# Performance work log

Measured on AMD Instinct MI355X. Metric: run time of the kernel, lower is better.

## Reference

```python
import jax, jax.numpy as jnp
import numpy as np
import math

L, B, T, S, D, H = 6, 4, 1024, 1024, 1024, 16
HD = D // H
SCALE = 1.0 / math.sqrt(HD)
EPS = 1e-5


def _ln(x, w, b):
    m = x.mean(-1, keepdims=True)
    v = ((x - m) ** 2).mean(-1, keepdims=True)
    return (x - m) * jax.lax.rsqrt(v + EPS) * w + b


def _mha(xq, xkv, qw, qb, kw, kb, vw, vb, ow, ob, mask):
    b, t, _ = xq.shape
    s = xkv.shape[1]
    q = (xq @ qw.T + qb).reshape(b, t, H, HD).transpose(0, 2, 1, 3)
    k = (xkv @ kw.T + kb).reshape(b, s, H, HD).transpose(0, 2, 1, 3)
    v = (xkv @ vw.T + vb).reshape(b, s, H, HD).transpose(0, 2, 1, 3)
    scores = jnp.einsum('bhqd,bhkd->bhqk', q, k) * SCALE
    scores = jnp.where(mask == 0, -jnp.inf, scores)
    attn = jax.nn.softmax(scores, axis=-1)  # dropout is identity (eval)
    o = jnp.einsum('bhqk,bhkd->bhqd', attn, v).transpose(0, 2, 1, 3).reshape(b, t, D)
    return o @ ow.T + ob


def _ffn(x, f1w, f1b, f2w, f2b, fnw, fnb):
    h = jax.nn.gelu(x @ f1w.T + f1b, approximate=False)
    y = h @ f2w.T + f2b
    return x + _ln(y, fnw, fnb)


def setup_inputs() -> dict:
    key = jax.random.key(0)
    ks = jax.random.split(key, 16)
    wf = lambda k: jax.random.normal(k, (L, D, D), jnp.float32) * 0.02
    zb = jnp.zeros((L, D), jnp.float32)
    ones = jnp.ones((L, D), jnp.float32)
    inp = {
        'x': jax.random.normal(ks[0], (B, T, D), jnp.float32),
        'enc_outputs': jax.random.normal(ks[1], (B, S, D), jnp.float32),
        'sqw': wf(ks[2]), 'sqb': zb, 'skw': wf(ks[3]), 'skb': zb,
        'svw': wf(ks[4]), 'svb': zb, 'sow': wf(ks[5]), 'sob': zb,
        'cqw': wf(ks[6]), 'cqb': zb, 'ckw': wf(ks[7]), 'ckb': zb,
        'cvw': wf(ks[8]), 'cvb': zb, 'cow': wf(ks[9]), 'cob': zb,
        'f1w': wf(ks[10]), 'f1b': zb, 'f2w': wf(ks[11]), 'f2b': zb,
        'fnw': ones, 'fnb': zb,
        'l1w': ones, 'l1b': zb, 'l2w': ones, 'l2b': zb, 'l3w': ones, 'l3b': zb,
        'src_mask': jnp.ones((1, 1, T, S), jnp.int32),
        'tgt_mask': jnp.tril(jnp.ones((T, T), jnp.int32))[None, None],
    }
    return inp


def reference(x, enc_outputs, sqw, sqb, skw, skb, svw, svb, sow, sob,
              cqw, cqb, ckw, ckb, cvw, cvb, cow, cob,
              f1w, f1b, f2w, f2b, fnw, fnb,
              l1w, l1b, l2w, l2b, l3w, l3b, src_mask, tgt_mask):
    for l in range(L):
        sa = _mha(x, x, sqw[l], sqb[l], skw[l], skb[l], svw[l], svb[l], sow[l], sob[l], tgt_mask)
        x = _ln(x + sa, l1w[l], l1b[l])
        ca = _mha(x, enc_outputs, cqw[l], cqb[l], ckw[l], ckb[l], cvw[l], cvb[l], cow[l], cob[l], src_mask)
        x = _ln(x + ca, l2w[l], l2b[l])
        ff = _ffn(x, f1w[l], f1b[l], f2w[l], f2b[l], fnw[l], fnb[l])
        x = _ln(x + ff, l3w[l], l3b[l])
    return x
```

## Files before the change

kernel.cpp:

```cpp
#include <hip/hip_runtime.h>
#include <stdint.h>

typedef unsigned short u16;
typedef unsigned int u32;
typedef __bf16 bf16x8 __attribute__((ext_vector_type(8)));
typedef float f32x4 __attribute__((ext_vector_type(4)));
typedef u16 u16x8 __attribute__((ext_vector_type(8)));
typedef u16 u16x4 __attribute__((ext_vector_type(4)));
typedef u32 u32x2 __attribute__((ext_vector_type(2)));

#define MFMA16(A, B, C) __builtin_amdgcn_mfma_f32_16x16x32_bf16((A), (B), (C), 0, 0, 0)

#define GLOAD_LDS16(GP, LP)                                                    \
  __builtin_amdgcn_global_load_lds(                                            \
      (__attribute__((address_space(1))) void*)(GP),                           \
      (__attribute__((address_space(3))) void*)(LP), 16, 0, 0)

__device__ __forceinline__ u16 f2bf(float f) {
  return __builtin_bit_cast(u16, (__bf16)f);
}

__device__ __forceinline__ float exp2_raw(float x) {
  float r;
  asm("v_exp_f32 %0, %1\n\ts_nop 0" : "=v"(r) : "v"(x));
  return r;
}

__device__ __forceinline__ float max3f(float a, float b, float c) {
  float d;
  asm("v_max3_f32 %0, %1, %2, %3" : "=v"(d) : "v"(a), "v"(b), "v"(c));
  return d;
}

__device__ __forceinline__ u32 cvt_pk_bf16(float lo, float hi) {
  u32 r;
  asm("v_cvt_pk_bf16_f32 %0, %1, %2" : "=v"(r) : "v"(lo), "v"(hi));
  return r;
}

#define SC2 0.1803368801111204f
#define DEFER_THR 11.541560327f

struct WPtrs {
  const float* p[10];
};

__global__ __launch_bounds__(256) void wcvt_kernel(WPtrs w, u16* __restrict__ dst, int loff) {
  const int idx = blockIdx.x * 256 + threadIdx.x;
  const int mat = idx >> 18;
  const int i = idx & 0x3FFFF;
  float4 v = ((const float4*)(w.p[mat] + loff))[i];
  u16x4 o = {f2bf(v.x), f2bf(v.y), f2bf(v.z), f2bf(v.w)};
  ((u16x4*)dst)[idx] = o;
}

struct GemmArgs {
  const u16* A[3];
  const u16* W[3];
  const float* bias[3];
  void* C[3];
  float scale[3];
};

template <int EPI>
__global__ __launch_bounds__(256, 3) void gemm_bt(GemmArgs g) {
  const int mat = blockIdx.y >> 3;
  const int n0 = (blockIdx.y & 7) * 128;
  const int m0 = blockIdx.x * 128;
  const int kz = blockIdx.z;
  const int kn = 16 / gridDim.z;
  const u16* __restrict__ A = g.A[mat];
  const u16* __restrict__ W = g.W[mat];

  __shared__ u16 As[128][64];
  __shared__ u16 Bs[128][64];

  const int tid = threadIdx.x;
  const int lane = tid & 63;
  const int wv = tid >> 6;
  const int wm = (wv >> 1) * 64;
  const int wn = (wv & 1) * 64;
  const int fr = lane & 15;
  const int fg = lane >> 4;

  f32x4 acc[4][4];
#pragma unroll
  for (int i = 0; i < 4; ++i)
#pragma unroll
    for (int j = 0; j < 4; ++j)
#pragma unroll
      for (int r = 0; r < 4; ++r) acc[i][j][r] = 0.f;

  const int row8 = lane >> 3;
  const int csw = ((lane & 7) ^ row8) * 8;
  const u16* ga = A + (size_t)(m0 + wv * 32 + row8) * 1024 + csw + kz * kn * 64;
  const u16* gb = W + (size_t)(n0 + wv * 32 + row8) * 1024 + csw + kz * kn * 64;

  for (int kt = 0; kt < kn; ++kt) {
    __syncthreads();
#pragma unroll
    for (int i = 0; i < 4; ++i) {
      GLOAD_LDS16(ga + (size_t)i * 8 * 1024, &As[wv * 32 + i * 8][0]);
      GLOAD_LDS16(gb + (size_t)i * 8 * 1024, &Bs[wv * 32 + i * 8][0]);
    }
    ga += 64;
    gb += 64;
    __syncthreads();
#pragma unroll
    for (int ks = 0; ks < 2; ++ks) {
      bf16x8 af[4], bfr[4];
#pragma unroll
      for (int i = 0; i < 4; ++i) {
        af[i] = *(const bf16x8*)&As[wm + i * 16 + fr][((ks * 4 + fg) ^ (fr & 7)) * 8];
        bfr[i] = *(const bf16x8*)&Bs[wn + i * 16 + fr][((ks * 4 + fg) ^ (fr & 7)) * 8];
      }
#pragma unroll
      for (int mi = 0; mi < 4; ++mi)
#pragma unroll
        for (int ni = 0; ni < 4; ++ni) acc[mi][ni] = MFMA16(af[mi], bfr[ni], acc[mi][ni]);
    }
  }

  const float* __restrict__ bias = g.bias[mat];
  const float scl = g.scale[mat];
  float bv[4];
#pragma unroll
  for (int ni = 0; ni < 4; ++ni) bv[ni] = (kz == 0) ? bias[n0 + wn + ni * 16 + fr] : 0.f;

#pragma unroll
  for (int mi = 0; mi < 4; ++mi) {
#pragma unroll
    for (int ni = 0; ni < 4; ++ni) {
      const int col = n0 + wn + ni * 16 + fr;
#pragma unroll
      for (int r = 0; r < 4; ++r) {
        const int row = m0 + wm + mi * 16 + fg * 4 + r;
        if (EPI == 1) {
          ((float*)g.C[mat] + (size_t)kz * (4096 * 1024))[(size_t)row * 1024 + col] =
              acc[mi][ni][r] + bv[ni];
        } else {
          float v = (acc[mi][ni][r] + bv[ni]) * scl;
          ((u16*)g.C[mat])[(size_t)row * 1024 + col] = f2bf(v);
        }
      }
    }
  }
}

__global__ __launch_bounds__(256, 4) void attn_fwd(const u16* __restrict__ Q,
                                                   const u16* __restrict__ K,
                                                   const u16* __restrict__ V,
                                                   u16* __restrict__ O, int causal) {
  const int b = blockIdx.x >> 4;
  const int h = blockIdx.x & 15;
  const int qb = causal ? (15 - blockIdx.y) : blockIdx.y;
  const int tid = threadIdx.x;
  const int lane = tid & 63;
  const int wv = tid >> 6;
  const int fr = lane & 15;
  const int fg = lane >> 4;

  __shared__ u16 Ks[2][64][64];
  __shared__ u16 Vt[2][64][64];
  __shared__ u16 Plds[4][16][64];

  const int qrow0 = b * 1024 + qb * 64 + wv * 16;
  const int col0 = h * 64;

  const u16* qp = Q + (size_t)(qrow0 + fr) * 1024 + col0 + fg * 8;
  bf16x8 aQ0 = *(const bf16x8*)qp;
  bf16x8 aQ1 = *(const bf16x8*)(qp + 32);

  f32x4 ov[4];
#pragma unroll
  for (int i = 0; i < 4; ++i)
#pragma unroll
    for (int r = 0; r < 4; ++r) ov[i][r] = 0.f;
  float m_run = -1e30f, l_part = 0.f;

  const int kv_base = b * 1024;
  const int qg = qb * 64 + wv * 16 + fr;
  const int nt = causal ? (qb + 1) : 16;

  const u16* gk0 = K + (size_t)(kv_base + wv * 16 + (lane >> 3)) * 1024 + col0 +
                   (((lane & 7) ^ (lane >> 3)) * 8);
  const int kkp = tid & 31;
  const int d0 = (tid >> 5) * 8;
  const u16* gv0 = V + (size_t)(kv_base + 2 * kkp) * 1024 + col0 + d0;

#define STAGE_K(T, BUF)                                                        \
  {                                                                            \
    const u16* gk = gk0 + (size_t)(T)*64 * 1024;                               \
    GLOAD_LDS16(gk, &Ks[BUF][wv * 16][0]);                                     \
    GLOAD_LDS16(gk + 8 * 1024, &Ks[BUF][wv * 16 + 8][0]);                      \
  }
#define LOAD_V(T)                                                              \
  {                                                                            \
    const u16* gvp = gv0 + (size_t)(T)*64 * 1024;                              \
    vr0 = *(const u16x8*)gvp;                                                  \
    vr1 = *(const u16x8*)(gvp + 1024);                                         \
  }
#define WRITE_V(BUF)                                                           \
  {                                                                            \
    _Pragma("unroll") for (int j = 0; j < 8; ++j) {                            \
      u32 pk = (u32)vr0[j] | ((u32)vr1[j] << 16);                              \
      *(u32*)&Vt[BUF][d0 + j][(((kkp >> 2) ^ j) * 8) + (kkp & 3) * 2] = pk;    \
    }                                                                          \
  }

  u16x8 vr0, vr1;
  STAGE_K(0, 0);
  LOAD_V(0);
  WRITE_V(0);

  for (int t = 0; t < nt; ++t) {
    const int cur = t & 1;
    __syncthreads();
    const bool pf = (t + 1 < nt);
    if (pf) {
      STAGE_K(t + 1, cur ^ 1);
      LOAD_V(t + 1);
    }

    f32x4 st[4];
    __builtin_amdgcn_s_setprio(1);
#pragma unroll
    for (int hh = 0; hh < 4; ++hh) {
#pragma unroll
      for (int r = 0; r < 4; ++r) st[hh][r] = 0.f;
      const u16* krow = &Ks[cur][hh * 16 + fr][0];
      bf16x8 k0 = *(const bf16x8*)(krow + ((fg ^ (fr & 7)) * 8));
      bf16x8 k1 = *(const bf16x8*)(krow + (((4 + fg) ^ (fr & 7)) * 8));
      st[hh] = MFMA16(k0, aQ0, st[hh]);
      st[hh] = MFMA16(k1, aQ1, st[hh]);
    }
    __builtin_amdgcn_s_setprio(0);

    if (causal && t == qb) {
#pragma unroll
      for (int hh = 0; hh < 4; ++hh)
#pragma unroll
        for (int r = 0; r < 4; ++r) {
          const int kkg = t * 64 + hh * 16 + fg * 4 + r;
          if (kkg > qg) st[hh][r] = -1e30f;
        }
    }

    float a = max3f(st[0][0], st[0][1], st[0][2]);
    a = max3f(a, st[0][3], st[1][0]);
    a = max3f(a, st[1][1], st[1][2]);
    a = max3f(a, st[1][3], st[2][0]);
    float bb = max3f(st[2][1], st[2][2], st[2][3]);
    bb = max3f(bb, st[3][0], st[3][1]);
    bb = max3f(bb, st[3][2], st[3][3]);
    const float tmax = fmaxf(a, bb);

    if (!__all(tmax <= m_run + DEFER_THR)) {
      float cm = fmaxf(tmax, __shfl_xor(tmax, 16));
      cm = fmaxf(cm, __shfl_xor(cm, 32));
      const float mnew = fmaxf(m_run, cm);
      const float fsc = exp2_raw(m_run - mnew);
      l_part *= fsc;
      float frs[4];
#pragma unroll
      for (int r = 0; r < 4; ++r) frs[r] = __shfl(fsc, fg * 4 + r);
#pragma unroll
      for (int dt = 0; dt < 4; ++dt)
#pragma unroll
        for (int r = 0; r < 4; ++r) ov[dt][r] *= frs[r];
      m_run = mnew;
    }

    float p[16];
#pragma unroll
    for (int hh = 0; hh < 4; ++hh)
#pragma unroll
      for (int r = 0; r < 4; ++r) {
        const float e = exp2_raw(st[hh][r] - m_run);
        p[hh * 4 + r] = e;
        l_part += e;
      }

#pragma unroll
    for (int hh = 0; hh < 4; ++hh) {
      u32x2 wpair = {cvt_pk_bf16(p[hh * 4 + 0], p[hh * 4 + 1]),
                     cvt_pk_bf16(p[hh * 4 + 2], p[hh * 4 + 3])};
      const int c = hh * 2 + (fg >> 1);
      *(u32x2*)&Plds[wv][fr][((c ^ (fr & 7)) * 8) + (fg & 1) * 4] = wpair;
    }
    bf16x8 pa[2];
#pragma unroll
    for (int ks = 0; ks < 2; ++ks)
      pa[ks] = *(const bf16x8*)&Plds[wv][fr][(((ks * 4 + fg) ^ (fr & 7)) * 8)];
    __builtin_amdgcn_s_setprio(1);
#pragma unroll
    for (int dt = 0; dt < 4; ++dt) {
#pragma unroll
      for (int ks = 0; ks < 2; ++ks) {
        bf16x8 bvv = *(const bf16x8*)&Vt[cur][dt * 16 + fr][(((ks * 4 + fg) ^ (fr & 7)) * 8)];
        ov[dt] = MFMA16(pa[ks], bvv, ov[dt]);
      }
    }
    __builtin_amdgcn_s_setprio(0);

    if (pf) WRITE_V(cur ^ 1);
  }

  float ps = l_part;
  ps += __shfl_xor(ps, 16);
  ps += __shfl_xor(ps, 32);
  const float linv = 1.0f / ps;
  float fin[4];
#pragma unroll
  for (int r = 0; r < 4; ++r) fin[r] = __shfl(linv, fg * 4 + r);
#pragma unroll
  for (int dt = 0; dt < 4; ++dt)
#pragma unroll
    for (int r = 0; r < 4; ++r) {
      const int row = qrow0 + fg * 4 + r;
      const int col = col0 + dt * 16 + fr;
      O[(size_t)row * 1024 + col] = f2bf(ov[dt][r] * fin[r]);
    }
#undef STAGE_K
#undef LOAD_V
#undef WRITE_V
}

__global__ __launch_bounds__(256) void ln_res_kernel(const float* __restrict__ X,
                                                     const float* __restrict__ T0,
                                                     const float* __restrict__ T1, int nT,
                                                     const float* __restrict__ w,
                                                     const float* __restrict__ bia,
                                                     float* __restrict__ Xo,
                                                     u16* __restrict__ Xb) {
  __shared__ float red[2][4];
  const int row = blockIdx.x;
  const int tid = threadIdx.x;
  const int lane = tid & 63, wv = tid >> 6;
  const size_t base = (size_t)row * 1024;
  float4 xv = ((const float4*)(X + base))[tid];
  float4 tv = ((const float4*)(T0 + base))[tid];
  float z0 = xv.x + tv.x, z1 = xv.y + tv.y, z2 = xv.z + tv.z, z3 = xv.w + tv.w;
  if (nT == 2) {
    float4 t1 = ((const float4*)(T1 + base))[tid];
    z0 += t1.x; z1 += t1.y; z2 += t1.z; z3 += t1.w;
  }
  float s = z0 + z1 + z2 + z3;
  float ss = z0 * z0 + z1 * z1 + z2 * z2 + z3 * z3;
#pragma unroll
  for (int m = 1; m <= 32; m <<= 1) {
    s += __shfl_xor(s, m);
    ss += __shfl_xor(ss, m);
  }
  if (lane == 0) {
    red[0][wv] = s;
    red[1][wv] = ss;
  }
  __syncthreads();
  s = red[0][0] + red[0][1] + red[0][2] + red[0][3];
  ss = red[1][0] + red[1][1] + red[1][2] + red[1][3];
  const float mean = s * (1.f / 1024.f);
  const float var = ss * (1.f / 1024.f) - mean * mean;
  const float rs = rsqrtf(fmaxf(var, 0.f) + 1e-5f);
  float4 wv4 = ((const float4*)w)[tid];
  float4 bv4 = ((const float4*)bia)[tid];
  float o0 = (z0 - mean) * rs * wv4.x + bv4.x;
  float o1 = (z1 - mean) * rs * wv4.y + bv4.y;
  float o2 = (z2 - mean) * rs * wv4.z + bv4.z;
  float o3 = (z3 - mean) * rs * wv4.w + bv4.w;
  ((float4*)(Xo + base))[tid] = make_float4(o0, o1, o2, o3);
  u16x4 ob = {f2bf(o0), f2bf(o1), f2bf(o2), f2bf(o3)};
  ((u16x4*)Xb)[base / 4 + tid] = ob;
}

__global__ __launch_bounds__(256) void ffn_ln_kernel(
    const float* __restrict__ X, const float* __restrict__ Y0, const float* __restrict__ Y1,
    int nT, const float* __restrict__ fw_, const float* __restrict__ fb_,
    const float* __restrict__ w3, const float* __restrict__ b3, float* __restrict__ Xo,
    u16* __restrict__ Xb) {
  __shared__ float red[2][4];
  const int row = blockIdx.x;
  const int tid = threadIdx.x;
  const int lane = tid & 63, wv = tid >> 6;
  const size_t base = (size_t)row * 1024;
  float4 yv = ((const float4*)(Y0 + base))[tid];
  if (nT == 2) {
    float4 y1 = ((const float4*)(Y1 + base))[tid];
    yv.x += y1.x; yv.y += y1.y; yv.z += y1.z; yv.w += y1.w;
  }
  float s = yv.x + yv.y + yv.z + yv.w;
  float ss = yv.x * yv.x + yv.y * yv.y + yv.z * yv.z + yv.w * yv.w;
#pragma unroll
  for (int m = 1; m <= 32; m <<= 1) {
    s += __shfl_xor(s, m);
    ss += __shfl_xor(ss, m);
  }
  if (lane == 0) {
    red[0][wv] = s;
    red[1][wv] = ss;
  }
  __syncthreads();
  s = red[0][0] + red[0][1] + red[0][2] + red[0][3];
  ss = red[1][0] + red[1][1] + red[1][2] + red[1][3];
  const float mean = s * (1.f / 1024.f);
  const float var = ss * (1.f / 1024.f) - mean * mean;
  const float rs = rsqrtf(fmaxf(var, 0.f) + 1e-5f);
  float4 xv = ((const float4*)(X + base))[tid];
  float4 fw4 = ((const float4*)fw_)[tid];
  float4 fb4 = ((const float4*)fb_)[tid];
  float z0 = 2.f * xv.x + (yv.x - mean) * rs * fw4.x + fb4.x;
  float z1 = 2.f * xv.y + (yv.y - mean) * rs * fw4.y + fb4.y;
  float z2 = 2.f * xv.z + (yv.z - mean) * rs * fw4.z + fb4.z;
  float z3 = 2.f * xv.w + (yv.w - mean) * rs * fw4.w + fb4.w;
  float s2 = z0 + z1 + z2 + z3;
  float ss2 = z0 * z0 + z1 * z1 + z2 * z2 + z3 * z3;
#pragma unroll
  for (int m = 1; m <= 32; m <<= 1) {
    s2 += __shfl_xor(s2, m);
    ss2 += __shfl_xor(ss2, m);
  }
  __syncthreads();
  if (lane == 0) {
    red[0][wv] = s2;
    red[1][wv] = ss2;
  }
  __syncthreads();
  s2 = red[0][0] + red[0][1] + red[0][2] + red[0][3];
  ss2 = red[1][0] + red[1][1] + red[1][2] + red[1][3];
  const float mean2 = s2 * (1.f / 1024.f);
  const float var2 = ss2 * (1.f / 1024.f) - mean2 * mean2;
  const float rs2 = rsqrtf(fmaxf(var2, 0.f) + 1e-5f);
  float4 w4 = ((const float4*)w3)[tid];
  float4 b4 = ((const float4*)b3)[tid];
  float o0 = (z0 - mean2) * rs2 * w4.x + b4.x;
  float o1 = (z1 - mean2) * rs2 * w4.y + b4.y;
  float o2 = (z2 - mean2) * rs2 * w4.z + b4.z;
  float o3 = (z3 - mean2) * rs2 * w4.w + b4.w;
  ((float4*)(Xo + base))[tid] = make_float4(o0, o1, o2, o3);
  u16x4 ob = {f2bf(o0), f2bf(o1), f2bf(o2), f2bf(o3)};
  ((u16x4*)Xb)[base / 4 + tid] = ob;
}

__global__ __launch_bounds__(256) void gelu_combine(const float* __restrict__ T0,
                                                    const float* __restrict__ T1, int nT,
                                                    u16* __restrict__ dst) {
  const size_t i = (size_t)blockIdx.x * 256 + threadIdx.x;
  float4 v = ((const float4*)T0)[i];
  if (nT == 2) {
    float4 u = ((const float4*)T1)[i];
    v.x += u.x; v.y += u.y; v.z += u.z; v.w += u.w;
  }
  v.x = 0.5f * v.x * (1.0f + erff(v.x * 0.70710678118654752f));
  v.y = 0.5f * v.y * (1.0f + erff(v.y * 0.70710678118654752f));
  v.z = 0.5f * v.z * (1.0f + erff(v.z * 0.70710678118654752f));
  v.w = 0.5f * v.w * (1.0f + erff(v.w * 0.70710678118654752f));
  u16x4 o = {f2bf(v.x), f2bf(v.y), f2bf(v.z), f2bf(v.w)};
  ((u16x4*)dst)[i] = o;
}

__global__ __launch_bounds__(256) void cast_kernel(const float* __restrict__ in,
                                                   u16* __restrict__ outb,
                                                   float* __restrict__ outf) {
  const size_t i = (size_t)blockIdx.x * 256 + threadIdx.x;
  float4 v = ((const float4*)in)[i];
  u16x4 o = {f2bf(v.x), f2bf(v.y), f2bf(v.z), f2bf(v.w)};
  ((u16x4*)outb)[i] = o;
  if (outf) ((float4*)outf)[i] = v;
}

extern "C" void kernel_launch(void* const* d_in, const int* in_sizes, int n_in, void* d_out,
                              int out_size, void* d_ws, size_t ws_size, hipStream_t stream) {
  const float* x_in = (const float*)d_in[0];
  const float* enc = (const float*)d_in[1];
  const float* sqw = (const float*)d_in[2];
  const float* sqb = (const float*)d_in[3];
  const float* skw = (const float*)d_in[4];
  const float* skb = (const float*)d_in[5];
  const float* svw = (const float*)d_in[6];
  const float* svb = (const float*)d_in[7];
  const float* sow = (const float*)d_in[8];
  const float* sob = (const float*)d_in[9];
  const float* cqw = (const float*)d_in[10];
  const float* cqb = (const float*)d_in[11];
  const float* ckw = (const float*)d_in[12];
  const float* ckb = (const float*)d_in[13];
  const float* cvw = (const float*)d_in[14];
  const float* cvb = (const float*)d_in[15];
  const float* cow = (const float*)d_in[16];
  const float* cob = (const float*)d_in[17];
  const float* f1w = (const float*)d_in[18];
  const float* f1b = (const float*)d_in[19];
  const float* f2w = (const float*)d_in[20];
  const float* f2b = (const float*)d_in[21];
  const float* fnw = (const float*)d_in[22];
  const float* fnb = (const float*)d_in[23];
  const float* l1w = (const float*)d_in[24];
  const float* l1b = (const float*)d_in[25];
  const float* l2w = (const float*)d_in[26];
  const float* l2b = (const float*)d_in[27];
  const float* l3w = (const float*)d_in[28];
  const float* l3b = (const float*)d_in[29];

  const size_t MB = 1024 * 1024;
  const int NS = (ws_size >= 108 * MB) ? 2 : 1;
  char* ws = (char*)d_ws;
  float* xf = (float*)ws;
  float* tmp = (float*)(ws + 16 * MB);
  char* p = ws + 16 * MB + (size_t)NS * 16 * MB;
  u16* xb = (u16*)p;   p += 8 * MB;
  u16* encb = (u16*)p; p += 8 * MB;
  u16* qbuf = (u16*)p; p += 8 * MB;
  u16* kbuf = (u16*)p; p += 8 * MB;
  u16* vbuf = (u16*)p; p += 8 * MB;
  u16* wbf = (u16*)p;
  float* tmp1 = tmp + (size_t)4 * 1024 * 1024;
  const size_t W1M = 1024 * 1024;

  cast_kernel<<<4096, 256, 0, stream>>>(x_in, xb, xf);
  cast_kernel<<<4096, 256, 0, stream>>>(enc, encb, nullptr);

  WPtrs wp;
  wp.p[0] = sqw; wp.p[1] = skw; wp.p[2] = svw; wp.p[3] = sow;
  wp.p[4] = cqw; wp.p[5] = ckw; wp.p[6] = cvw; wp.p[7] = cow;
  wp.p[8] = f1w; wp.p[9] = f2w;

  for (int l = 0; l < 6; ++l) {
    const int loff = l * (int)W1M;
    const size_t bo = (size_t)l * 1024;
    wcvt_kernel<<<10240, 256, 0, stream>>>(wp, wbf, loff);

    GemmArgs g;
    g.scale[0] = SC2; g.scale[1] = 1.f; g.scale[2] = 1.f;
    g.A[0] = xb; g.A[1] = xb; g.A[2] = xb;
    g.W[0] = wbf; g.W[1] = wbf + W1M; g.W[2] = wbf + 2 * W1M;
    g.bias[0] = sqb + bo; g.bias[1] = skb + bo; g.bias[2] = svb + bo;
    g.C[0] = qbuf; g.C[1] = kbuf; g.C[2] = vbuf;
    gemm_bt<0><<<dim3(32, 24, 1), 256, 0, stream>>>(g);
    attn_fwd<<<dim3(64, 16), 256, 0, stream>>>(qbuf, kbuf, vbuf, qbuf, 1);
    g.scale[0] = 1.f;
    g.A[0] = qbuf; g.W[0] = wbf + 3 * W1M; g.bias[0] = sob + bo; g.C[0] = tmp;
    gemm_bt<1><<<dim3(32, 8, NS), 256, 0, stream>>>(g);
    ln_res_kernel<<<4096, 256, 0, stream>>>(xf, tmp, tmp1, NS, l1w + bo, l1b + bo, xf, xb);

    g.scale[0] = SC2;
    g.A[0] = xb; g.A[1] = encb; g.A[2] = encb;
    g.W[0] = wbf + 4 * W1M; g.W[1] = wbf + 5 * W1M; g.W[2] = wbf + 6 * W1M;
    g.bias[0] = cqb + bo; g.bias[1] = ckb + bo; g.bias[2] = cvb + bo;
    g.C[0] = qbuf; g.C[1] = kbuf; g.C[2] = vbuf;
    gemm_bt<0><<<dim3(32, 24, 1), 256, 0, stream>>>(g);
    attn_fwd<<<dim3(64, 16), 256, 0, stream>>>(qbuf, kbuf, vbuf, qbuf, 0);
    g.scale[0] = 1.f;
    g.A[0] = qbuf; g.W[0] = wbf + 7 * W1M; g.bias[0] = cob + bo; g.C[0] = tmp;
    gemm_bt<1><<<dim3(32, 8, NS), 256, 0, stream>>>(g);
    ln_res_kernel<<<4096, 256, 0, stream>>>(xf, tmp, tmp1, NS, l2w + bo, l2b + bo, xf, xb);

    g.A[0] = xb; g.W[0] = wbf + 8 * W1M; g.bias[0] = f1b + bo; g.C[0] = tmp;
    gemm_bt<1><<<dim3(32, 8, NS), 256, 0, stream>>>(g);
    gelu_combine<<<4096, 256, 0, stream>>>(tmp, tmp1, NS, kbuf);
    g.A[0] = kbuf; g.W[0] = wbf + 9 * W1M; g.bias[0] = f2b + bo; g.C[0] = tmp;
    gemm_bt<1><<<dim3(32, 8, NS), 256, 0, stream>>>(g);
    float* xo = (l == 5) ? (float*)d_out : xf;
    ffn_ln_kernel<<<4096, 256, 0, stream>>>(xf, tmp, tmp1, NS, fnw + bo, fnb + bo, l3w + bo,
                                            l3b + bo, xo, xb);
  }
}
```

Baseline: 1.499 ms.

## Store GEMM partials in bf16, hoist weight conversion, widen attention blocks

GEMM split-K partial outputs are now written as bf16 instead of fp32, and the layernorm, GELU and FFN kernels read bf16 partials, halving intermediate traffic. When the workspace is large enough, all layers' weights are converted to bf16 in one launch up front rather than once per layer. Attention blocks grow to 512 threads covering 128 query rows. The first 4 waves stage K and the upper 256 threads load V, and the causal mask is applied to the last two tiles. GEMM occupancy is raised to 4 blocks. Rounding the split-K partials to bf16 before summation costs accuracy before the residual add and layernorm.

Result: faster. 1.424 ms (-5.0%).

```diff
diff --git a/kernel.cpp b/kernel.cpp
--- a/kernel.cpp
+++ b/kernel.cpp
@@ -20,6 +20,10 @@
   return __builtin_bit_cast(u16, (__bf16)f);
 }
 
+__device__ __forceinline__ float bf2f(u16 v) {
+  return __builtin_bit_cast(float, ((u32)v) << 16);
+}
+
 __device__ __forceinline__ float exp2_raw(float x) {
   float r;
   asm("v_exp_f32 %0, %1\n\ts_nop 0" : "=v"(r) : "v"(x));
@@ -45,10 +49,11 @@
   const float* p[10];
 };
 
-__global__ __launch_bounds__(256) void wcvt_kernel(WPtrs w, u16* __restrict__ dst, int loff) {
+__global__ __launch_bounds__(256) void wcvt_kernel(WPtrs w, u16* __restrict__ dst, int loff,
+                                                   int perMat) {
   const int idx = blockIdx.x * 256 + threadIdx.x;
-  const int mat = idx >> 18;
-  const int i = idx & 0x3FFFF;
+  const int mat = idx / perMat;
+  const int i = idx - mat * perMat;
   float4 v = ((const float4*)(w.p[mat] + loff))[i];
   u16x4 o = {f2bf(v.x), f2bf(v.y), f2bf(v.z), f2bf(v.w)};
   ((u16x4*)dst)[idx] = o;
@@ -58,12 +63,11 @@
   const u16* A[3];
   const u16* W[3];
   const float* bias[3];
-  void* C[3];
+  u16* C[3];
   float scale[3];
 };
 
-template <int EPI>
-__global__ __launch_bounds__(256, 3) void gemm_bt(GemmArgs g) {
+__global__ __launch_bounds__(256, 4) void gemm_bt(GemmArgs g) {
   const int mat = blockIdx.y >> 3;
   const int n0 = (blockIdx.y & 7) * 128;
   const int m0 = blockIdx.x * 128;
@@ -127,6 +131,7 @@
 #pragma unroll
   for (int ni = 0; ni < 4; ++ni) bv[ni] = (kz == 0) ? bias[n0 + wn + ni * 16 + fr] : 0.f;
 
+  u16* __restrict__ C = g.C[mat] + (size_t)kz * (4096 * 1024);
 #pragma unroll
   for (int mi = 0; mi < 4; ++mi) {
 #pragma unroll
@@ -135,25 +140,19 @@
 #pragma unroll
       for (int r = 0; r < 4; ++r) {
         const int row = m0 + wm + mi * 16 + fg * 4 + r;
-        if (EPI == 1) {
-          ((float*)g.C[mat] + (size_t)kz * (4096 * 1024))[(size_t)row * 1024 + col] =
-              acc[mi][ni][r] + bv[ni];
-        } else {
-          float v = (acc[mi][ni][r] + bv[ni]) * scl;
-          ((u16*)g.C[mat])[(size_t)row * 1024 + col] = f2bf(v);
-        }
+        C[(size_t)row * 1024 + col] = f2bf((acc[mi][ni][r] + bv[ni]) * scl);
       }
     }
   }
 }
 
-__global__ __launch_bounds__(256, 4) void attn_fwd(const u16* __restrict__ Q,
+__global__ __launch_bounds__(512, 4) void attn_fwd(const u16* __restrict__ Q,
                                                    const u16* __restrict__ K,
                                                    const u16* __restrict__ V,
                                                    u16* __restrict__ O, int causal) {
   const int b = blockIdx.x >> 4;
   const int h = blockIdx.x & 15;
-  const int qb = causal ? (15 - blockIdx.y) : blockIdx.y;
+  const int qb = causal ? (7 - blockIdx.y) : blockIdx.y;
   const int tid = threadIdx.x;
   const int lane = tid & 63;
   const int wv = tid >> 6;
@@ -162,9 +161,9 @@
 
   __shared__ u16 Ks[2][64][64];
   __shared__ u16 Vt[2][64][64];
-  __shared__ u16 Plds[4][16][64];
-
-  const int qrow0 = b * 1024 + qb * 64 + wv * 16;
+  __shared__ u16 Plds[8][16][64];
+
+  const int qrow0 = b * 1024 + qb * 128 + wv * 16;
   const int col0 = h * 64;
 
   const u16* qp = Q + (size_t)(qrow0 + fr) * 1024 + col0 + fg * 8;
@@ -179,29 +178,30 @@
   float m_run = -1e30f, l_part = 0.f;
 
   const int kv_base = b * 1024;
-  const int qg = qb * 64 + wv * 16 + fr;
-  const int nt = causal ? (qb + 1) : 16;
+  const int qg = qb * 128 + wv * 16 + fr;
+  const int nt = causal ? (2 * qb + 2) : 16;
 
   const u16* gk0 = K + (size_t)(kv_base + wv * 16 + (lane >> 3)) * 1024 + col0 +
                    (((lane & 7) ^ (lane >> 3)) * 8);
-  const int kkp = tid & 31;
-  const int d0 = (tid >> 5) * 8;
+  const int vt = tid - 256;
+  const int kkp = vt & 31;
+  const int d0 = (vt >> 5) * 8;
   const u16* gv0 = V + (size_t)(kv_base + 2 * kkp) * 1024 + col0 + d0;
 
 #define STAGE_K(T, BUF)                                                        \
-  {                                                                            \
+  if (wv < 4) {                                                                \
     const u16* gk = gk0 + (size_t)(T)*64 * 1024;                               \
     GLOAD_LDS16(gk, &Ks[BUF][wv * 16][0]);                                     \
     GLOAD_LDS16(gk + 8 * 1024, &Ks[BUF][wv * 16 + 8][0]);                      \
   }
 #define LOAD_V(T)                                                              \
-  {                                                                            \
+  if (tid >= 256) {                                                            \
     const u16* gvp = gv0 + (size_t)(T)*64 * 1024;                              \
     vr0 = *(const u16x8*)gvp;                                                  \
     vr1 = *(const u16x8*)(gvp + 1024);                                         \
   }
 #define WRITE_V(BUF)                                                           \
-  {                                                                            \
+  if (tid >= 256) {                                                            \
     _Pragma("unroll") for (int j = 0; j < 8; ++j) {                            \
       u32 pk = (u32)vr0[j] | ((u32)vr1[j] << 16);                              \
       *(u32*)&Vt[BUF][d0 + j][(((kkp >> 2) ^ j) * 8) + (kkp & 3) * 2] = pk;    \
@@ -236,7 +236,7 @@
     }
     __builtin_amdgcn_s_setprio(0);
 
-    if (causal && t == qb) {
+    if (causal && t >= 2 * qb) {
 #pragma unroll
       for (int hh = 0; hh < 4; ++hh)
 #pragma unroll
@@ -326,9 +326,14 @@
 #undef WRITE_V
 }
 
+__device__ __forceinline__ float4 ld_bf4(const u16* p, size_t idx4) {
+  u16x4 t = ((const u16x4*)p)[idx4];
+  return make_float4(bf2f(t[0]), bf2f(t[1]), bf2f(t[2]), bf2f(t[3]));
+}
+
 __global__ __launch_bounds__(256) void ln_res_kernel(const float* __restrict__ X,
-                                                     const float* __restrict__ T0,
-                                                     const float* __restrict__ T1, int nT,
+                                                     const u16* __restrict__ T0,
+                                                     const u16* __restrict__ T1, int nT,
                                                      const float* __restrict__ w,
                                                      const float* __restrict__ bia,
                                                      float* __restrict__ Xo,
@@ -339,10 +344,10 @@
   const int lane = tid & 63, wv = tid >> 6;
   const size_t base = (size_t)row * 1024;
   float4 xv = ((const float4*)(X + base))[tid];
-  float4 tv = ((const float4*)(T0 + base))[tid];
+  float4 tv = ld_bf4(T0, base / 4 + tid);
   float z0 = xv.x + tv.x, z1 = xv.y + tv.y, z2 = xv.z + tv.z, z3 = xv.w + tv.w;
   if (nT == 2) {
-    float4 t1 = ((const float4*)(T1 + base))[tid];
+    float4 t1 = ld_bf4(T1, base / 4 + tid);
     z0 += t1.x; z1 += t1.y; z2 += t1.z; z3 += t1.w;
   }
   float s = z0 + z1 + z2 + z3;
@@ -374,7 +379,7 @@
 }
 
 __global__ __launch_bounds__(256) void ffn_ln_kernel(
-    const float* __restrict__ X, const float* __restrict__ Y0, const float* __restrict__ Y1,
+    const float* __restrict__ X, const u16* __restrict__ Y0, const u16* __restrict__ Y1,
     int nT, const float* __restrict__ fw_, const float* __restrict__ fb_,
     const float* __restrict__ w3, const float* __restrict__ b3, float* __restrict__ Xo,
     u16* __restrict__ Xb) {
@@ -383,9 +388,9 @@
   const int tid = threadIdx.x;
   const int lane = tid & 63, wv = tid >> 6;
   const size_t base = (size_t)row * 1024;
-  float4 yv = ((const float4*)(Y0 + base))[tid];
+  float4 yv = ld_bf4(Y0, base / 4 + tid);
   if (nT == 2) {
-    float4 y1 = ((const float4*)(Y1 + base))[tid];
+    float4 y1 = ld_bf4(Y1, base / 4 + tid);
     yv.x += y1.x; yv.y += y1.y; yv.z += y1.z; yv.w += y1.w;
   }
   float s = yv.x + yv.y + yv.z + yv.w;
@@ -441,13 +446,13 @@
   ((u16x4*)Xb)[base / 4 + tid] = ob;
 }
 
-__global__ __launch_bounds__(256) void gelu_combine(const float* __restrict__ T0,
-                                                    const float* __restrict__ T1, int nT,
+__global__ __launch_bounds__(256) void gelu_combine(const u16* __restrict__ T0,
+                                                    const u16* __restrict__ T1, int nT,
                                                     u16* __restrict__ dst) {
   const size_t i = (size_t)blockIdx.x * 256 + threadIdx.x;
-  float4 v = ((const float4*)T0)[i];
+  float4 v = ld_bf4(T0, i);
   if (nT == 2) {
-    float4 u = ((const float4*)T1)[i];
+    float4 u = ld_bf4(T1, i);
     v.x += u.x; v.y += u.y; v.z += u.z; v.w += u.w;
   }
   v.x = 0.5f * v.x * (1.0f + erff(v.x * 0.70710678118654752f));
@@ -502,18 +507,19 @@
   const float* l3b = (const float*)d_in[29];
 
   const size_t MB = 1024 * 1024;
+  const int ALLW = (ws_size >= 210 * MB) ? 1 : 0;
   const int NS = (ws_size >= 108 * MB) ? 2 : 1;
   char* ws = (char*)d_ws;
   float* xf = (float*)ws;
-  float* tmp = (float*)(ws + 16 * MB);
-  char* p = ws + 16 * MB + (size_t)NS * 16 * MB;
+  u16* tmpb = (u16*)(ws + 16 * MB);
+  char* p = ws + 16 * MB + (size_t)NS * 8 * MB;
   u16* xb = (u16*)p;   p += 8 * MB;
   u16* encb = (u16*)p; p += 8 * MB;
   u16* qbuf = (u16*)p; p += 8 * MB;
   u16* kbuf = (u16*)p; p += 8 * MB;
   u16* vbuf = (u16*)p; p += 8 * MB;
   u16* wbf = (u16*)p;
-  float* tmp1 = tmp + (size_t)4 * 1024 * 1024;
+  u16* tmpb1 = tmpb + (size_t)4 * 1024 * 1024;
   const size_t W1M = 1024 * 1024;
 
   cast_kernel<<<4096, 256, 0, stream>>>(x_in, xb, xf);
@@ -524,43 +530,46 @@
   wp.p[4] = cqw; wp.p[5] = ckw; wp.p[6] = cvw; wp.p[7] = cow;
   wp.p[8] = f1w; wp.p[9] = f2w;
 
+  if (ALLW) wcvt_kernel<<<61440, 256, 0, stream>>>(wp, wbf, 0, 6 * 262144);
+
   for (int l = 0; l < 6; ++l) {
-    const int loff = l * (int)W1M;
     const size_t bo = (size_t)l * 1024;
-    wcvt_kernel<<<10240, 256, 0, stream>>>(wp, wbf, loff);
+    if (!ALLW) wcvt_kernel<<<10240, 256, 0, stream>>>(wp, wbf, l * (int)W1M, 262144);
+    #define WT(t) (ALLW ? (wbf + ((size_t)(t)*6 + l) * W1M) : (wbf + (size_t)(t)*W1M))
 
     GemmArgs g;
     g.scale[0] = SC2; g.scale[1] = 1.f; g.scale[2] = 1.f;
     g.A[0] = xb; g.A[1] = xb; g.A[2] = xb;
-    g.W[0] = wbf; g.W[1] = wbf + W1M; g.W[2] = wbf + 2 * W1M;
+    g.W[0] = WT(0); g.W[1] = WT(1); g.W[2] = WT(2);
     g.bias[0] = sqb + bo; g.bias[1] = skb + bo; g.bias[2] = svb + bo;
     g.C[0] = qbuf; g.C[1] = kbuf; g.C[2] = vbuf;
-    gemm_bt<0><<<dim3(32, 24, 1), 256, 0, stream>>>(g);
-    attn_fwd<<<dim3(64, 16), 256, 0, stream>>>(qbuf, kbuf, vbuf, qbuf, 1);
+    gemm_bt<<<dim3(32, 24, 1), 256, 0, stream>>>(g);
+    attn_fwd<<<dim3(64, 8), 512, 0, stream>>>(qbuf, kbuf, vbuf, qbuf, 1);
     g.scale[0] = 1.f;
-    g.A[0] = qbuf; g.W[0] = wbf + 3 * W1M; g.bias[0] = sob + bo; g.C[0] = tmp;
-    gemm_bt<1><<<dim3(32, 8, NS), 256, 0, stream>>>(g);
-    ln_res_kernel<<<4096, 256, 0, stream>>>(xf, tmp, tmp1, NS, l1w + bo, l1b + bo, xf, xb);
+    g.A[0] = qbuf; g.W[0] = WT(3); g.bias[0] = sob + bo; g.C[0] = tmpb;
+    gemm_bt<<<dim3(32, 8, NS), 256, 0, stream>>>(g);
+    ln_res_kernel<<<4096, 256, 0, stream>>>(xf, tmpb, tmpb1, NS, l1w + bo, l1b + bo, xf, xb);
 
     g.scale[0] = SC2;
     g.A[0] = xb; g.A[1] = encb; g.A[2] = encb;
-    g.W[0] = wbf + 4 * W1M; g.W[1] = wbf + 5 * W1M; g.W[2] = wbf + 6 * W1M;
+    g.W[0] = WT(4); g.W[1] = WT(5); g.W[2] = WT(6);
     g.bias[0] = cqb + bo; g.bias[1] = ckb + bo; g.bias[2] = cvb + bo;
     g.C[0] = qbuf; g.C[1] = kbuf; g.C[2] = vbuf;
-    gemm_bt<0><<<dim3(32, 24, 1), 256, 0, stream>>>(g);
-    attn_fwd<<<dim3(64, 16), 256, 0, stream>>>(qbuf, kbuf, vbuf, qbuf, 0);
+    gemm_bt<<<dim3(32, 24, 1), 256, 0, stream>>>(g);
+    attn_fwd<<<dim3(64, 8), 512, 0, stream>>>(qbuf, kbuf, vbuf, qbuf, 0);
     g.scale[0] = 1.f;
-    g.A[0] = qbuf; g.W[0] = wbf + 7 * W1M; g.bias[0] = cob + bo; g.C[0] = tmp;
-    gemm_bt<1><<<dim3(32, 8, NS), 256, 0, stream>>>(g);
-    ln_res_kernel<<<4096, 256, 0, stream>>>(xf, tmp, tmp1, NS, l2w + bo, l2b + bo, xf, xb);
-
-    g.A[0] = xb; g.W[0] = wbf + 8 * W1M; g.bias[0] = f1b + bo; g.C[0] = tmp;
-    gemm_bt<1><<<dim3(32, 8, NS), 256, 0, stream>>>(g);
-    gelu_combine<<<4096, 256, 0, stream>>>(tmp, tmp1, NS, kbuf);
-    g.A[0] = kbuf; g.W[0] = wbf + 9 * W1M; g.bias[0] = f2b + bo; g.C[0] = tmp;
-    gemm_bt<1><<<dim3(32, 8, NS), 256, 0, stream>>>(g);
+    g.A[0] = qbuf; g.W[0] = WT(7); g.bias[0] = cob + bo; g.C[0] = tmpb;
+    gemm_bt<<<dim3(32, 8, NS), 256, 0, stream>>>(g);
+    ln_res_kernel<<<4096, 256, 0, stream>>>(xf, tmpb, tmpb1, NS, l2w + bo, l2b + bo, xf, xb);
+
+    g.A[0] = xb; g.W[0] = WT(8); g.bias[0] = f1b + bo; g.C[0] = tmpb;
+    gemm_bt<<<dim3(32, 8, NS), 256, 0, stream>>>(g);
+    gelu_combine<<<4096, 256, 0, stream>>>(tmpb, tmpb1, NS, kbuf);
+    g.A[0] = kbuf; g.W[0] = WT(9); g.bias[0] = f2b + bo; g.C[0] = tmpb;
+    gemm_bt<<<dim3(32, 8, NS), 256, 0, stream>>>(g);
     float* xo = (l == 5) ? (float*)d_out : xf;
-    ffn_ln_kernel<<<4096, 256, 0, stream>>>(xf, tmp, tmp1, NS, fnw + bo, fnb + bo, l3w + bo,
+    ffn_ln_kernel<<<4096, 256, 0, stream>>>(xf, tmpb, tmpb1, NS, fnw + bo, fnb + bo, l3w + bo,
                                             l3b + bo, xo, xb);
-  }
-}
+    #undef WT
+  }
+}
```
